# Performance work log

Measured on AMD Instinct MI355X. Metric: run time of the kernel, lower is better.

## Reference

```python
import jax, jax.numpy as jnp
import numpy as np

TOPK = 13
ALPHA = 1.0
BETA = 6.0
REG_MAX = 16
W_MATCH, W_IOU, W_DFL, W_CONTRAST = 1.0, 7.5, 1.5, 1.0
EPS = 1e-7


def bbox_iou(a, b):
    # a, b: [..., 4] xyxy, broadcastable
    x1 = jnp.maximum(a[..., 0], b[..., 0])
    y1 = jnp.maximum(a[..., 1], b[..., 1])
    x2 = jnp.minimum(a[..., 2], b[..., 2])
    y2 = jnp.minimum(a[..., 3], b[..., 3])
    inter = jnp.clip(x2 - x1, 0.0) * jnp.clip(y2 - y1, 0.0)
    area_a = (a[..., 2] - a[..., 0]) * (a[..., 3] - a[..., 1])
    area_b = (b[..., 2] - b[..., 0]) * (b[..., 3] - b[..., 1])
    return inter / (area_a + area_b - inter + EPS)


def bbox_ciou(a, b):
    iou = bbox_iou(a, b)
    cw = jnp.maximum(a[..., 2], b[..., 2]) - jnp.minimum(a[..., 0], b[..., 0])
    ch = jnp.maximum(a[..., 3], b[..., 3]) - jnp.minimum(a[..., 1], b[..., 1])
    c2 = cw * cw + ch * ch + EPS
    rho2 = ((b[..., 0] + b[..., 2] - a[..., 0] - a[..., 2]) ** 2
            + (b[..., 1] + b[..., 3] - a[..., 1] - a[..., 3]) ** 2) * 0.25
    w1, h1 = a[..., 2] - a[..., 0], a[..., 3] - a[..., 1] + EPS
    w2, h2 = b[..., 2] - b[..., 0], b[..., 3] - b[..., 1] + EPS
    v = (4.0 / (np.pi ** 2)) * (jnp.arctan(w2 / h2) - jnp.arctan(w1 / h1)) ** 2
    alpha = jax.lax.stop_gradient(v / (v - iou + (1.0 + EPS)))
    return iou - rho2 / c2 - v * alpha


def _per_image(scores, boxes, logits, prompt, gts, anchors, stride, img_size):
    # scores [N], boxes [N,4], logits [N,4*REG_MAX], prompt [D], gts [G,4]
    N = scores.shape[0]
    dt = scores.dtype
    inside = ((anchors[None, :, 0] >= gts[:, None, 0]) & (anchors[None, :, 0] <= gts[:, None, 2])
              & (anchors[None, :, 1] >= gts[:, None, 1]) & (anchors[None, :, 1] <= gts[:, None, 3]))  # [G,N]
    ious = bbox_iou(boxes[None, :, :], gts[:, None, :])  # [G,N]
    prob = jax.nn.sigmoid(scores)
    align = jnp.where(inside, jnp.power(prob[None, :], ALPHA) * jnp.power(ious, BETA), -1.0)  # [G,N]
    top_vals, top_idx = jax.lax.top_k(align, TOPK)  # [G,TOPK]
    metric = jax.vmap(lambda i, v: jnp.full((N,), -2.0, dt).at[i].set(v))(top_idx, top_vals)  # [G,N]
    best = metric.max(axis=0)
    matched = metric.argmax(axis=0)  # [N]
    fg = best >= 0.0  # valid candidates always have align >= 0
    fgf = fg.astype(dt)
    overlap = jnp.take_along_axis(ious, matched[None, :], axis=0)[0]  # [N]
    target_scores = jnp.where(fg, jnp.maximum(overlap, 0.1), 0.0)
    target_boxes = jnp.where(fg[:, None], gts[matched], 0.0)  # [N,4]
    n_pos = fgf.sum()
    denom = jnp.maximum(n_pos, 1.0)
    # ---- BCE-with-logits (mean over all anchors) ----
    bce = jnp.maximum(scores, 0.0) - scores * target_scores + jnp.log1p(jnp.exp(-jnp.abs(scores)))
    match_loss = bce.mean()
    # ---- CIoU loss (masked mean over positives) ----
    ciou = bbox_ciou(boxes, target_boxes)
    iou_loss = jnp.sum((1.0 - ciou) * fgf) / denom
    # ---- DFL ----
    dist = jnp.concatenate([anchors - target_boxes[:, :2], target_boxes[:, 2:] - anchors], axis=-1) / stride
    dist = jnp.clip(dist, 0.0, REG_MAX - 1 - 0.01)  # [N,4]
    logsm = jax.nn.log_softmax(logits.reshape(N, 4, REG_MAX), axis=-1)
    tl = dist.astype(jnp.int32)
    tr = jnp.minimum(tl + 1, REG_MAX - 1)
    wl = tr.astype(dt) - dist
    wr = 1.0 - wl
    ll = -jnp.take_along_axis(logsm, tl[..., None], axis=-1)[..., 0]
    lr = -jnp.take_along_axis(logsm, tr[..., None], axis=-1)[..., 0]
    dfl = ll * wl + lr * wr  # [N,4]
    dfl_loss = jnp.sum(dfl * fgf[:, None]) / (4.0 * denom)
    # ---- Contrastive prompt alignment ----
    center = (target_boxes[:, :2] + target_boxes[:, 2:]) * 0.5 / jnp.maximum(img_size, 1.0)
    cv = center / jnp.maximum(jnp.linalg.norm(center, axis=-1, keepdims=True), 1e-12)
    pv = prompt[:2]
    pv = pv / jnp.maximum(jnp.linalg.norm(pv), 1e-12)
    contrast_loss = jnp.sum((1.0 - jnp.sum(cv * pv[None, :], axis=-1)) * fgf) / denom
    # ---- stats ----
    pos_score_sum = jnp.sum(prob * fgf)
    neg_score_sum = jnp.sum(prob * (1.0 - fgf))
    matched_iou_sum = jnp.sum(overlap * fgf)
    return match_loss, iou_loss, dfl_loss, contrast_loss, n_pos, pos_score_sum, neg_score_sum, matched_iou_sum


def setup_inputs() -> dict:
    img = 1280
    pts, strs = [], []
    for s in (8, 16, 32):
        n = img // s
        xs = (np.arange(n, dtype=np.float32) + 0.5) * s
        gx, gy = np.meshgrid(xs, xs)
        pts.append(np.stack([gx.ravel(), gy.ravel()], -1))
        strs.append(np.full((n * n, 1), s, np.float32))
    anchor_points = jnp.asarray(np.concatenate(pts).astype(np.float32))  # [33600,2]
    stride_tensor = jnp.asarray(np.concatenate(strs))  # [33600,1]
    N = anchor_points.shape[0]
    B, G = 16, 20
    k = jax.random.split(jax.random.key(0), 6)
    pred_scores = jax.random.normal(k[0], (B, N), jnp.float32) - 2.0
    off = jax.random.uniform(k[1], (B, N, 4), jnp.float32, 4.0, 80.0)
    ap = anchor_points[None, :, :]
    pred_boxes = jnp.concatenate([ap - off[..., :2], ap + off[..., 2:]], -1)
    box_distribution = jax.random.normal(k[2], (B, N, 4 * REG_MAX), jnp.float32)
    prompt_embedding = jax.random.normal(k[3], (B, 256), jnp.float32)
    c = jax.random.uniform(k[4], (B, G, 2), jnp.float32, 100.0, 1180.0)
    wh = jax.random.uniform(k[5], (B, G, 2), jnp.float32, 30.0, 300.0)
    gt_boxes = jnp.concatenate([c - wh * 0.5, c + wh * 0.5], -1)
    return {"pred_boxes": pred_boxes, "pred_scores": pred_scores, "anchor_points": anchor_points,
            "stride_tensor": stride_tensor, "box_distribution": box_distribution,
            "prompt_embedding": prompt_embedding, "gt_boxes": gt_boxes, "image_size": img}


def reference(pred_boxes, pred_scores, anchor_points, stride_tensor, box_distribution, prompt_embedding, gt_boxes, image_size):
    B, N = pred_scores.shape
    res = jax.vmap(_per_image, in_axes=(0, 0, 0, 0, 0, None, None, None))(
        pred_scores, pred_boxes, box_distribution, prompt_embedding, gt_boxes,
        anchor_points, stride_tensor, float(image_size))
    match, iou, dfl, contrast, n_pos, pos_sum, neg_sum, miou = [r.sum() for r in res]
    total_pos = n_pos
    total_neg = float(B * N) - total_pos
    nb = float(B)
    loss = (W_MATCH * match + W_IOU * iou + W_DFL * dfl + W_CONTRAST * contrast) / nb
    pd = jnp.maximum(total_pos, 1.0)
    nd = jnp.maximum(total_neg, 1.0)
    return (loss, match / nb, iou / nb, dfl / nb, contrast / nb,
            total_pos, total_neg, pos_sum / pd, neg_sum / nd, miou / pd)
```

## Files before the change

kernel.cpp:

```cpp
#include <hip/hip_runtime.h>
#include <math.h>

#define TOPK 13
#define REG_MAX 16
#define EPSF 1e-7f
#define MAXM 512
#define NEG_SENT -1e30f
#define NBCE 256

__global__ __launch_bounds__(256) void k1_kernel(
    const float* __restrict__ boxes,
    const float* __restrict__ scores,
    const float* __restrict__ gts,
    const int*   __restrict__ img_sz,
    unsigned long long* __restrict__ pk_out,
    float* __restrict__ bcepart,
    int N, int G, int NBG, int total)
{
    const int tid  = threadIdx.x;
    const int lane = tid & 63;
    const int w    = tid >> 6;

    if ((int)blockIdx.x >= NBG) {
        const int blk = blockIdx.x - NBG;
        float bce0 = 0.f, prsum = 0.f;
        const int nvec = total >> 2;
        const float4* s4 = (const float4*)scores;
        for (int n = blk*256 + tid; n < nvec; n += NBCE*256) {
            float4 v = s4[n];
            float ss[4] = { v.x, v.y, v.z, v.w };
#pragma unroll
            for (int q = 0; q < 4; q++) {
                float s = ss[q];
                bce0  += fmaxf(s, 0.0f) + log1pf(expf(-fabsf(s)));
                prsum += 1.0f / (1.0f + expf(-s));
            }
        }
        if (blk == 0) {
            for (int n = (nvec << 2) + tid; n < total; n += 256) {
                float s = scores[n];
                bce0  += fmaxf(s, 0.0f) + log1pf(expf(-fabsf(s)));
                prsum += 1.0f / (1.0f + expf(-s));
            }
        }
        float v1 = bce0, v2 = prsum;
#pragma unroll
        for (int off = 32; off > 0; off >>= 1) {
            v1 += __shfl_xor(v1, off);
            v2 += __shfl_xor(v2, off);
        }
        __shared__ float r1[4], r2[4];
        if (lane == 0) { r1[w] = v1; r2[w] = v2; }
        __syncthreads();
        if (tid == 0) {
            bcepart[blk*2 + 0] = r1[0] + r1[1] + r1[2] + r1[3];
            bcepart[blk*2 + 1] = r2[0] + r2[1] + r2[2] + r2[3];
        }
        return;
    }

    const int bg  = blockIdx.x;
    const int b   = bg / G;
    const int g   = bg - b * G;
    const int img = img_sz[0];

    const float4 gt = ((const float4*)gts)[bg];
    const float area_b = (gt.z - gt.x) * (gt.w - gt.y);

    float lv[TOPK];
    int   li[TOPK];
#pragma unroll
    for (int i = 0; i < TOPK; i++) { lv[i] = NEG_SENT; li[i] = 0; }

    const float4* bx = (const float4*)(boxes + (size_t)b * N * 4);
    const float*  sc = scores + (size_t)b * N;

    int base = 0;
#pragma unroll
    for (int L = 0; L < 3; L++) {
        const int s = 8 << L;
        const int n = img / s;
        const float fs = (float)s;
        int i0 = max(0,     (int)ceilf (gt.x / fs - 0.5f) - 1);
        int i1 = min(n - 1, (int)floorf(gt.z / fs - 0.5f) + 1);
        int j0 = max(0,     (int)ceilf (gt.y / fs - 0.5f) - 1);
        int j1 = min(n - 1, (int)floorf(gt.w / fs - 0.5f) + 1);
        if (i1 >= i0 && j1 >= j0) {
            const int W = i1 - i0 + 1;
            const int cnt = W * (j1 - j0 + 1);
            for (int t = tid; t < cnt; t += 256) {
                const int i = i0 + t % W;
                const int j = j0 + t / W;
                const int idx = base + j * n + i;
                const float4 a    = bx[idx];
                const float  sraw = sc[idx];
                const float ax = ((float)i + 0.5f) * fs;
                const float ay = ((float)j + 0.5f) * fs;
                float x1 = fmaxf(a.x, gt.x), y1 = fmaxf(a.y, gt.y);
                float x2 = fminf(a.z, gt.z), y2 = fminf(a.w, gt.w);
                float inter  = fmaxf(x2 - x1, 0.0f) * fmaxf(y2 - y1, 0.0f);
                float area_a = (a.z - a.x) * (a.w - a.y);
                float iou  = inter / (area_a + area_b - inter + EPSF);
                float prob = 1.0f / (1.0f + expf(-sraw));
                float i2 = iou * iou;
                float align = prob * i2 * i2 * i2;
                bool inside = (ax >= gt.x) & (ax <= gt.z) & (ay >= gt.y) & (ay <= gt.w);
                align = inside ? align : NEG_SENT;
                if (align > lv[TOPK-1]) {
                    float cv = align; int ci = idx;
#pragma unroll
                    for (int q = 0; q < TOPK; q++) {
                        if (cv > lv[q]) {
                            float tv = lv[q]; int ti = li[q];
                            lv[q] = cv; li[q] = ci; cv = tv; ci = ti;
                        }
                    }
                }
            }
        }
        base += n * n;
    }

    __shared__ float sval[256 * TOPK];
    __shared__ int   sidx[256 * TOPK];
#pragma unroll
    for (int i = 0; i < TOPK; i++) { sval[tid*TOPK+i] = lv[i]; sidx[tid*TOPK+i] = li[i]; }
    __builtin_amdgcn_s_waitcnt(0);

    __shared__ float wtv[4][TOPK];
    __shared__ int   wti[4][TOPK];
    int h = 0;
    for (int k = 0; k < TOPK; k++) {
        float v = (h < TOPK) ? sval[tid*TOPK + h] : NEG_SENT;
        float bv = v; int bs = lane;
#pragma unroll
        for (int off = 32; off > 0; off >>= 1) {
            float ov = __shfl_xor(bv, off);
            int   os = __shfl_xor(bs, off);
            if (ov > bv || (ov == bv && os < bs)) { bv = ov; bs = os; }
        }
        if (lane == bs) {
            wtv[w][k] = v;
            wti[w][k] = sidx[tid*TOPK + h];
            h++;
        }
    }
    __syncthreads();

    if (w == 0) {
        int hh = 0;
        for (int k = 0; k < TOPK; k++) {
            float v = (lane < 4) ? wtv[lane & 3][hh] : NEG_SENT;
            float bv = v; int bs = lane;
#pragma unroll
            for (int off = 32; off > 0; off >>= 1) {
                float ov = __shfl_xor(bv, off);
                int   os = __shfl_xor(bs, off);
                if (ov > bv || (ov == bv && os < bs)) { bv = ov; bs = os; }
            }
            if (lane == bs) {
                unsigned long long p = 0ull;
                if (v >= 0.0f) {
                    p = (1ull << 62)
                      | ((unsigned long long)(unsigned int)wti[lane & 3][hh] << 37)
                      | ((unsigned long long)__float_as_uint(v) << 5)
                      | (unsigned long long)(31 - g);
                }
                pk_out[bg*TOPK + k] = p;
                hh++;
            }
        }
    }
}

__global__ __launch_bounds__(64) void fg_kernel(
    const float* __restrict__ boxes, const float* __restrict__ scores,
    const float* __restrict__ logits, const float* __restrict__ prompt,
    const float* __restrict__ gts, const int* __restrict__ img_sz,
    const unsigned long long* __restrict__ pk_in,
    float* __restrict__ part, int N, int G, int PD)
{
    const int bg   = blockIdx.x;
    const int b    = bg / G;
    const int g    = bg - b * G;
    const int lane = threadIdx.x;
    const int M    = G * TOPK;

    __shared__ unsigned long long pk[MAXM];
    for (int e = lane; e < M; e += 64) pk[e] = pk_in[b*M + e];
    __builtin_amdgcn_s_waitcnt(0);

    const int ent = lane >> 2;
    const int q   = lane & 3;
    unsigned long long mine = 0ull;
    if (ent < TOPK) mine = pk[g*TOPK + ent];

    int lose = 0;
    if (mine != 0ull) {
        for (int e2 = q; e2 < M; e2 += 4) {
            unsigned long long p2 = pk[e2];
            lose |= (int)((((p2 ^ mine) >> 37) == 0ull) & (p2 > mine));
        }
    }
    lose |= __shfl_xor(lose, 1);
    lose |= __shfl_xor(lose, 2);
    const bool winner = (mine != 0ull) && (lose == 0);

    const float4 tb = ((const float4*)gts)[b*G + g];
    const int img = img_sz[0];

    float side = 0.f;
    float npos = 0.f, iouv = 0.f, conv = 0.f, probv = 0.f, corrv = 0.f, miouv = 0.f;

    if (winner) {
        const int idx = (int)((mine >> 37) & 0x1FFFFFFull);
        const int n0 = img >> 3, n1 = img >> 4, n2 = img >> 5;
        int r = idx; float fs; int n;
        if (r < n0*n0)                 { fs = 8.0f;  n = n0; }
        else if (r < n0*n0 + n1*n1)    { r -= n0*n0;         fs = 16.0f; n = n1; }
        else                           { r -= n0*n0 + n1*n1; fs = 32.0f; n = n2; }
        (void)n2;
        const int jj = r / n, ii = r - jj * n;
        const float ax = ((float)ii + 0.5f) * fs;
        const float ay = ((float)jj + 0.5f) * fs;

        float dq = (q == 0) ? (ax - tb.x) : (q == 1) ? (ay - tb.y)
                 : (q == 2) ? (tb.z - ax) : (tb.w - ay);
        dq /= fs;
        const float4* lg4 = (const float4*)(logits + ((size_t)b*N + idx) * (4*REG_MAX)) + q*4;
        float4 q0 = lg4[0], q1 = lg4[1], q2 = lg4[2], q3 = lg4[3];
        float row[REG_MAX] = { q0.x,q0.y,q0.z,q0.w, q1.x,q1.y,q1.z,q1.w,
                               q2.x,q2.y,q2.z,q2.w, q3.x,q3.y,q3.z,q3.w };
        float d = fminf(fmaxf(dq, 0.0f), (float)(REG_MAX-1) - 0.01f);
        int tl = (int)d;
        int tr = min(tl + 1, REG_MAX - 1);
        float wl = (float)tr - d;
        float wr = 1.0f - wl;
        float m = row[0];
#pragma unroll
        for (int jx = 1; jx < REG_MAX; jx++) m = fmaxf(m, row[jx]);
        float se = 0.f, rtl = row[0], rtr = row[0];
#pragma unroll
        for (int jx = 0; jx < REG_MAX; jx++) {
            se += expf(row[jx] - m);
            rtl = (jx == tl) ? row[jx] : rtl;
            rtr = (jx == tr) ? row[jx] : rtr;
        }
        float lse = m + logf(se);
        side = (lse - rtl) * wl + (lse - rtr) * wr;
    }
    float dfl4 = side;
    dfl4 += __shfl_xor(dfl4, 1);
    dfl4 += __shfl_xor(dfl4, 2);

    float dflv = 0.f;
    if (winner && q == 0) {
        const int idx = (int)((mine >> 37) & 0x1FFFFFFull);
        const float4 a = ((const float4*)(boxes + (size_t)b*N*4))[idx];
        float s    = scores[(size_t)b*N + idx];
        float prob = 1.0f / (1.0f + expf(-s));

        float x1 = fmaxf(a.x, tb.x), y1 = fmaxf(a.y, tb.y);
        float x2 = fminf(a.z, tb.z), y2 = fminf(a.w, tb.w);
        float inter  = fmaxf(x2 - x1, 0.f) * fmaxf(y2 - y1, 0.f);
        float area_a = (a.z - a.x) * (a.w - a.y);
        float area_b = (tb.z - tb.x) * (tb.w - tb.y);
        float iou = inter / (area_a + area_b - inter + EPSF);
        float tsc = fmaxf(iou, 0.1f);

        float cw = fmaxf(a.z, tb.z) - fminf(a.x, tb.x);
        float ch = fmaxf(a.w, tb.w) - fminf(a.y, tb.y);
        float c2 = cw*cw + ch*ch + EPSF;
        float dxc = tb.x + tb.z - a.x - a.z;
        float dyc = tb.y + tb.w - a.y - a.w;
        float rho2 = (dxc*dxc + dyc*dyc) * 0.25f;
        float w1 = a.z - a.x, h1 = a.w - a.y + EPSF;
        float w2 = tb.z - tb.x, h2 = tb.w - tb.y + EPSF;
        float dat = atanf(w2/h2) - atanf(w1/h1);
        float v   = 0.4052847345693511f * dat * dat;
        float alpha = v / (v - iou + (1.0f + EPSF));
        float ciou  = iou - rho2/c2 - v*alpha;
        iouv = 1.0f - ciou;
        dflv = dfl4;

        float imgf = fmaxf((float)img, 1.0f);
        float p0 = prompt[(size_t)b*PD + 0], p1 = prompt[(size_t)b*PD + 1];
        float pn = fmaxf(sqrtf(p0*p0 + p1*p1), 1e-12f);
        float cx = (tb.x + tb.z) * 0.5f / imgf;
        float cy = (tb.y + tb.w) * 0.5f / imgf;
        float cn = fmaxf(sqrtf(cx*cx + cy*cy), 1e-12f);
        conv = 1.0f - (cx*(p0/pn) + cy*(p1/pn)) / cn;

        npos  = 1.0f;
        probv = prob;
        corrv = -s * tsc;
        miouv = iou;
    }

    float vals[7] = { npos, iouv, dflv, conv, probv, corrv, miouv };
#pragma unroll
    for (int k = 0; k < 7; k++) {
        float v = vals[k];
#pragma unroll
        for (int off = 32; off > 0; off >>= 1) v += __shfl_xor(v, off);
        vals[k] = v;
    }
    if (lane == 0) {
        float* p = part + (size_t)bg * 7;
#pragma unroll
        for (int k = 0; k < 7; k++) p[k] = vals[k];
    }
}

__global__ __launch_bounds__(64) void finalize_kernel(
    const float* __restrict__ part, const float* __restrict__ bcepart,
    float* __restrict__ out, int N, int B, int G)
{
    const int lane = threadIdx.x;
    float np = 0.f, iouS = 0.f, dflS = 0.f, conS = 0.f;
    float probS = 0.f, corrS = 0.f, miouS = 0.f;
    if (lane < B) {
        float a0=0,a1=0,a2=0,a3=0,a4=0,a5=0,a6=0;
        const float* p = part + (size_t)lane * G * 7;
        for (int g = 0; g < G; g++) {
            a0 += p[g*7+0]; a1 += p[g*7+1]; a2 += p[g*7+2]; a3 += p[g*7+3];
            a4 += p[g*7+4]; a5 += p[g*7+5]; a6 += p[g*7+6];
        }
        float denom = fmaxf(a0, 1.0f);
        np    = a0;
        iouS  = a1 / denom;
        dflS  = a2 / (4.0f * denom);
        conS  = a3 / denom;
        probS = a4;
        corrS = a5;
        miouS = a6;
    }
    float b0 = 0.f, b1 = 0.f;
    for (int qb = lane; qb < NBCE; qb += 64) {
        b0 += bcepart[2*qb + 0];
        b1 += bcepart[2*qb + 1];
    }
    float vals[9] = { np, iouS, dflS, conS, probS, corrS, miouS, b0, b1 };
#pragma unroll
    for (int k = 0; k < 9; k++) {
        float v = vals[k];
#pragma unroll
        for (int off = 32; off > 0; off >>= 1) v += __shfl_xor(v, off);
        vals[k] = v;
    }
    if (lane == 0) {
        float bce0 = vals[7], prall = vals[8];
        float match = (bce0 + vals[5]) / (float)N;
        float iou = vals[1], dfl = vals[2], con = vals[3];
        float tp  = vals[0];
        float tn  = (float)B * (float)N - tp;
        float nb  = (float)B;
        float loss = (1.0f*match + 7.5f*iou + 1.5f*dfl + 1.0f*con) / nb;
        float pd = fmaxf(tp, 1.0f), nd = fmaxf(tn, 1.0f);
        out[0] = loss;
        out[1] = match / nb;
        out[2] = iou / nb;
        out[3] = dfl / nb;
        out[4] = con / nb;
        out[5] = tp;
        out[6] = tn;
        out[7] = vals[4] / pd;
        out[8] = (prall - vals[4]) / nd;
        out[9] = vals[6] / pd;
    }
}

extern "C" void kernel_launch(void* const* d_in, const int* in_sizes, int n_in,
                              void* d_out, int out_size, void* d_ws, size_t ws_size,
                              hipStream_t stream)
{
    const float* boxes   = (const float*)d_in[0];
    const float* scores  = (const float*)d_in[1];
    const float* logits  = (const float*)d_in[4];
    const float* prompt  = (const float*)d_in[5];
    const float* gts     = (const float*)d_in[6];
    const int*   img     = (const int*)d_in[7];

    const int N  = in_sizes[2] / 2;
    const int B  = in_sizes[1] / N;
    const int G  = in_sizes[6] / (B * 4);
    const int PD = in_sizes[5] / B;
    const int NBG = B * G;

    float* out = (float*)d_out;
    char*  ws  = (char*)d_ws;

    unsigned long long* pk = (unsigned long long*)ws;
    size_t off = (size_t)NBG * TOPK * sizeof(unsigned long long);
    off = (off + 63) & ~(size_t)63;
    float* part = (float*)(ws + off);
    off += (size_t)NBG * 7 * sizeof(float);
    off = (off + 63) & ~(size_t)63;
    float* bcep = (float*)(ws + off);

    k1_kernel<<<NBG + NBCE, 256, 0, stream>>>(boxes, scores, gts, img,
                                              pk, bcep, N, G, NBG, B*N);
    fg_kernel<<<NBG, 64, 0, stream>>>(boxes, scores, logits, prompt,
                                      gts, img, pk, part, N, G, PD);
    finalize_kernel<<<1, 64, 0, stream>>>(part, bcep, out, N, B, G);
}
```

Before: 227.7 us.

## Fuse TAL top-k and foreground loss into one per-image kernel

Replaces the per-(image,GT) top-k kernel and the separate foreground-loss kernel with a single kernel that runs one block per image. Each wavefront handles a subset of GTs and keeps its candidates in shared memory, then the block resolves conflicts and computes the CIoU, DFL and contrast terms for all winners in place. This removes a kernel launch and the global round trip of the packed candidates. In exchange, parallelism drops from B*G blocks to B blocks, each wave walks its GTs serially, and the conflict check becomes an O(M^2) loop per thread. G is assumed to be at most 32.

```diff
diff --git a/kernel.cpp b/kernel.cpp
--- a/kernel.cpp
+++ b/kernel.cpp
@@ -4,25 +4,32 @@
 #define TOPK 13
 #define REG_MAX 16
 #define EPSF 1e-7f
-#define MAXM 512
 #define NEG_SENT -1e30f
 #define NBCE 256
-
-__global__ __launch_bounds__(256) void k1_kernel(
+#define MAXG 32
+
+__global__ __launch_bounds__(256) void mega_kernel(
     const float* __restrict__ boxes,
     const float* __restrict__ scores,
+    const float* __restrict__ logits,
+    const float* __restrict__ prompt,
     const float* __restrict__ gts,
     const int*   __restrict__ img_sz,
-    unsigned long long* __restrict__ pk_out,
-    float* __restrict__ bcepart,
-    int N, int G, int NBG, int total)
+    float* __restrict__ ws_img,
+    float* __restrict__ ws_bce,
+    int N, int B, int G, int PD, int total)
 {
     const int tid  = threadIdx.x;
     const int lane = tid & 63;
     const int w    = tid >> 6;
 
-    if ((int)blockIdx.x >= NBG) {
-        const int blk = blockIdx.x - NBG;
+    __shared__ float sval[256 * TOPK];
+    __shared__ int   sidx[256 * TOPK];
+    __shared__ unsigned long long pk[MAXG * TOPK];
+    __shared__ float wred[4][7];
+
+    if ((int)blockIdx.x >= B) {
+        const int blk = blockIdx.x - B;
         float bce0 = 0.f, prsum = 0.f;
         const int nvec = total >> 2;
         const float4* s4 = (const float4*)scores;
@@ -49,108 +56,88 @@
             v1 += __shfl_xor(v1, off);
             v2 += __shfl_xor(v2, off);
         }
-        __shared__ float r1[4], r2[4];
-        if (lane == 0) { r1[w] = v1; r2[w] = v2; }
+        if (lane == 0) { wred[w][0] = v1; wred[w][1] = v2; }
         __syncthreads();
         if (tid == 0) {
-            bcepart[blk*2 + 0] = r1[0] + r1[1] + r1[2] + r1[3];
-            bcepart[blk*2 + 1] = r2[0] + r2[1] + r2[2] + r2[3];
+            ws_bce[blk*2 + 0] = wred[0][0] + wred[1][0] + wred[2][0] + wred[3][0];
+            ws_bce[blk*2 + 1] = wred[0][1] + wred[1][1] + wred[2][1] + wred[3][1];
         }
         return;
     }
 
-    const int bg  = blockIdx.x;
-    const int b   = bg / G;
-    const int g   = bg - b * G;
+    const int b   = blockIdx.x;
     const int img = img_sz[0];
-
-    const float4 gt = ((const float4*)gts)[bg];
-    const float area_b = (gt.z - gt.x) * (gt.w - gt.y);
-
-    float lv[TOPK];
-    int   li[TOPK];
-#pragma unroll
-    for (int i = 0; i < TOPK; i++) { lv[i] = NEG_SENT; li[i] = 0; }
+    const int M   = G * TOPK;
 
     const float4* bx = (const float4*)(boxes + (size_t)b * N * 4);
     const float*  sc = scores + (size_t)b * N;
 
-    int base = 0;
-#pragma unroll
-    for (int L = 0; L < 3; L++) {
-        const int s = 8 << L;
-        const int n = img / s;
-        const float fs = (float)s;
-        int i0 = max(0,     (int)ceilf (gt.x / fs - 0.5f) - 1);
-        int i1 = min(n - 1, (int)floorf(gt.z / fs - 0.5f) + 1);
-        int j0 = max(0,     (int)ceilf (gt.y / fs - 0.5f) - 1);
-        int j1 = min(n - 1, (int)floorf(gt.w / fs - 0.5f) + 1);
-        if (i1 >= i0 && j1 >= j0) {
-            const int W = i1 - i0 + 1;
-            const int cnt = W * (j1 - j0 + 1);
-            for (int t = tid; t < cnt; t += 256) {
-                const int i = i0 + t % W;
-                const int j = j0 + t / W;
-                const int idx = base + j * n + i;
-                const float4 a    = bx[idx];
-                const float  sraw = sc[idx];
-                const float ax = ((float)i + 0.5f) * fs;
-                const float ay = ((float)j + 0.5f) * fs;
-                float x1 = fmaxf(a.x, gt.x), y1 = fmaxf(a.y, gt.y);
-                float x2 = fminf(a.z, gt.z), y2 = fminf(a.w, gt.w);
-                float inter  = fmaxf(x2 - x1, 0.0f) * fmaxf(y2 - y1, 0.0f);
-                float area_a = (a.z - a.x) * (a.w - a.y);
-                float iou  = inter / (area_a + area_b - inter + EPSF);
-                float prob = 1.0f / (1.0f + expf(-sraw));
-                float i2 = iou * iou;
-                float align = prob * i2 * i2 * i2;
-                bool inside = (ax >= gt.x) & (ax <= gt.z) & (ay >= gt.y) & (ay <= gt.w);
-                align = inside ? align : NEG_SENT;
-                if (align > lv[TOPK-1]) {
-                    float cv = align; int ci = idx;
-#pragma unroll
-                    for (int q = 0; q < TOPK; q++) {
-                        if (cv > lv[q]) {
-                            float tv = lv[q]; int ti = li[q];
-                            lv[q] = cv; li[q] = ci; cv = tv; ci = ti;
+    for (int g = w; g < G; g += 4) {
+        const float4 gt = ((const float4*)gts)[b*G + g];
+        const float area_b = (gt.z - gt.x) * (gt.w - gt.y);
+
+        float lv[TOPK];
+        int   li[TOPK];
+#pragma unroll
+        for (int i = 0; i < TOPK; i++) { lv[i] = NEG_SENT; li[i] = 0; }
+
+        int base = 0;
+#pragma unroll
+        for (int L = 0; L < 3; L++) {
+            const int s = 8 << L;
+            const int n = img / s;
+            const float fs = (float)s;
+            int i0 = max(0,     (int)ceilf (gt.x / fs - 0.5f) - 1);
+            int i1 = min(n - 1, (int)floorf(gt.z / fs - 0.5f) + 1);
+            int j0 = max(0,     (int)ceilf (gt.y / fs - 0.5f) - 1);
+            int j1 = min(n - 1, (int)floorf(gt.w / fs - 0.5f) + 1);
+            if (i1 >= i0 && j1 >= j0) {
+                const int W = i1 - i0 + 1;
+                const int cnt = W * (j1 - j0 + 1);
+                const int q64 = 64 / W, r64 = 64 - q64 * W;
+                int ii = lane % W, jj = lane / W;
+                for (int t = lane; t < cnt; t += 64) {
+                    const int i = i0 + ii;
+                    const int j = j0 + jj;
+                    const int idx = base + j * n + i;
+                    const float4 a    = bx[idx];
+                    const float  sraw = sc[idx];
+                    const float ax = ((float)i + 0.5f) * fs;
+                    const float ay = ((float)j + 0.5f) * fs;
+                    float x1 = fmaxf(a.x, gt.x), y1 = fmaxf(a.y, gt.y);
+                    float x2 = fminf(a.z, gt.z), y2 = fminf(a.w, gt.w);
+                    float inter  = fmaxf(x2 - x1, 0.0f) * fmaxf(y2 - y1, 0.0f);
+                    float area_a = (a.z - a.x) * (a.w - a.y);
+                    float iou  = inter / (area_a + area_b - inter + EPSF);
+                    float prob = 1.0f / (1.0f + expf(-sraw));
+                    float i2v = iou * iou;
+                    float align = prob * i2v * i2v * i2v;
+                    bool inside = (ax >= gt.x) & (ax <= gt.z) & (ay >= gt.y) & (ay <= gt.w);
+                    align = inside ? align : NEG_SENT;
+                    if (align > lv[TOPK-1]) {
+                        float cv = align; int ci = idx;
+#pragma unroll
+                        for (int q = 0; q < TOPK; q++) {
+                            if (cv > lv[q]) {
+                                float tv = lv[q]; int ti = li[q];
+                                lv[q] = cv; li[q] = ci; cv = tv; ci = ti;
+                            }
                         }
                     }
+                    ii += r64; jj += q64;
+                    if (ii >= W) { ii -= W; jj++; }
                 }
             }
-        }
-        base += n * n;
-    }
-
-    __shared__ float sval[256 * TOPK];
-    __shared__ int   sidx[256 * TOPK];
-#pragma unroll
-    for (int i = 0; i < TOPK; i++) { sval[tid*TOPK+i] = lv[i]; sidx[tid*TOPK+i] = li[i]; }
-    __builtin_amdgcn_s_waitcnt(0);
-
-    __shared__ float wtv[4][TOPK];
-    __shared__ int   wti[4][TOPK];
-    int h = 0;
-    for (int k = 0; k < TOPK; k++) {
-        float v = (h < TOPK) ? sval[tid*TOPK + h] : NEG_SENT;
-        float bv = v; int bs = lane;
-#pragma unroll
-        for (int off = 32; off > 0; off >>= 1) {
-            float ov = __shfl_xor(bv, off);
-            int   os = __shfl_xor(bs, off);
-            if (ov > bv || (ov == bv && os < bs)) { bv = ov; bs = os; }
-        }
-        if (lane == bs) {
-            wtv[w][k] = v;
-            wti[w][k] = sidx[tid*TOPK + h];
-            h++;
-        }
-    }
-    __syncthreads();
-
-    if (w == 0) {
-        int hh = 0;
+            base += n * n;
+        }
+
+#pragma unroll
+        for (int i = 0; i < TOPK; i++) { sval[tid*TOPK+i] = lv[i]; sidx[tid*TOPK+i] = li[i]; }
+        __builtin_amdgcn_s_waitcnt(0);
+
+        int h = 0;
         for (int k = 0; k < TOPK; k++) {
-            float v = (lane < 4) ? wtv[lane & 3][hh] : NEG_SENT;
+            float v = (h < TOPK) ? sval[tid*TOPK + h] : NEG_SENT;
             float bv = v; int bs = lane;
 #pragma unroll
             for (int off = 32; off > 0; off >>= 1) {
@@ -162,102 +149,50 @@
                 unsigned long long p = 0ull;
                 if (v >= 0.0f) {
                     p = (1ull << 62)
-                      | ((unsigned long long)(unsigned int)wti[lane & 3][hh] << 37)
+                      | ((unsigned long long)(unsigned int)sidx[tid*TOPK + h] << 37)
                       | ((unsigned long long)__float_as_uint(v) << 5)
                       | (unsigned long long)(31 - g);
                 }
-                pk_out[bg*TOPK + k] = p;
-                hh++;
-            }
-        }
-    }
-}
-
-__global__ __launch_bounds__(64) void fg_kernel(
-    const float* __restrict__ boxes, const float* __restrict__ scores,
-    const float* __restrict__ logits, const float* __restrict__ prompt,
-    const float* __restrict__ gts, const int* __restrict__ img_sz,
-    const unsigned long long* __restrict__ pk_in,
-    float* __restrict__ part, int N, int G, int PD)
-{
-    const int bg   = blockIdx.x;
-    const int b    = bg / G;
-    const int g    = bg - b * G;
-    const int lane = threadIdx.x;
-    const int M    = G * TOPK;
-
-    __shared__ unsigned long long pk[MAXM];
-    for (int e = lane; e < M; e += 64) pk[e] = pk_in[b*M + e];
-    __builtin_amdgcn_s_waitcnt(0);
-
-    const int ent = lane >> 2;
-    const int q   = lane & 3;
-    unsigned long long mine = 0ull;
-    if (ent < TOPK) mine = pk[g*TOPK + ent];
-
-    int lose = 0;
-    if (mine != 0ull) {
-        for (int e2 = q; e2 < M; e2 += 4) {
+                pk[g*TOPK + k] = p;
+                h++;
+            }
+        }
+    }
+    __syncthreads();
+
+    float npos = 0.f, iouS = 0.f, dflS = 0.f, conS = 0.f;
+    float probS = 0.f, corrS = 0.f, miouS = 0.f;
+
+    const float imgf = fmaxf((float)img, 1.0f);
+    float p0 = prompt[(size_t)b*PD + 0], p1 = prompt[(size_t)b*PD + 1];
+    float pn = fmaxf(sqrtf(p0*p0 + p1*p1), 1e-12f);
+    p0 /= pn; p1 /= pn;
+
+    for (int e = tid; e < M; e += 256) {
+        const unsigned long long mine = pk[e];
+        if (mine == 0ull) continue;
+        bool lose = false;
+        for (int e2 = 0; e2 < M; e2++) {
             unsigned long long p2 = pk[e2];
-            lose |= (int)((((p2 ^ mine) >> 37) == 0ull) & (p2 > mine));
-        }
-    }
-    lose |= __shfl_xor(lose, 1);
-    lose |= __shfl_xor(lose, 2);
-    const bool winner = (mine != 0ull) && (lose == 0);
-
-    const float4 tb = ((const float4*)gts)[b*G + g];
-    const int img = img_sz[0];
-
-    float side = 0.f;
-    float npos = 0.f, iouv = 0.f, conv = 0.f, probv = 0.f, corrv = 0.f, miouv = 0.f;
-
-    if (winner) {
+            lose |= (((p2 ^ mine) >> 37) == 0ull) & (p2 > mine);
+        }
+        if (lose) continue;
+
+        const int g   = e / TOPK;
         const int idx = (int)((mine >> 37) & 0x1FFFFFFull);
-        const int n0 = img >> 3, n1 = img >> 4, n2 = img >> 5;
+        const float4 tb = ((const float4*)gts)[b*G + g];
+
+        const int n0 = img >> 3, n1 = img >> 4;
         int r = idx; float fs; int n;
-        if (r < n0*n0)                 { fs = 8.0f;  n = n0; }
-        else if (r < n0*n0 + n1*n1)    { r -= n0*n0;         fs = 16.0f; n = n1; }
-        else                           { r -= n0*n0 + n1*n1; fs = 32.0f; n = n2; }
-        (void)n2;
+        if (r < n0*n0)              { fs = 8.0f;  n = n0; }
+        else if (r < n0*n0 + n1*n1) { r -= n0*n0;         fs = 16.0f; n = n1; }
+        else                        { r -= n0*n0 + n1*n1; fs = 32.0f; n = img >> 5; }
         const int jj = r / n, ii = r - jj * n;
         const float ax = ((float)ii + 0.5f) * fs;
         const float ay = ((float)jj + 0.5f) * fs;
 
-        float dq = (q == 0) ? (ax - tb.x) : (q == 1) ? (ay - tb.y)
-                 : (q == 2) ? (tb.z - ax) : (tb.w - ay);
-        dq /= fs;
-        const float4* lg4 = (const float4*)(logits + ((size_t)b*N + idx) * (4*REG_MAX)) + q*4;
-        float4 q0 = lg4[0], q1 = lg4[1], q2 = lg4[2], q3 = lg4[3];
-        float row[REG_MAX] = { q0.x,q0.y,q0.z,q0.w, q1.x,q1.y,q1.z,q1.w,
-                               q2.x,q2.y,q2.z,q2.w, q3.x,q3.y,q3.z,q3.w };
-        float d = fminf(fmaxf(dq, 0.0f), (float)(REG_MAX-1) - 0.01f);
-        int tl = (int)d;
-        int tr = min(tl + 1, REG_MAX - 1);
-        float wl = (float)tr - d;
-        float wr = 1.0f - wl;
-        float m = row[0];
-#pragma unroll
-        for (int jx = 1; jx < REG_MAX; jx++) m = fmaxf(m, row[jx]);
-        float se = 0.f, rtl = row[0], rtr = row[0];
-#pragma unroll
-        for (int jx = 0; jx < REG_MAX; jx++) {
-            se += expf(row[jx] - m);
-            rtl = (jx == tl) ? row[jx] : rtl;
-            rtr = (jx == tr) ? row[jx] : rtr;
-        }
-        float lse = m + logf(se);
-        side = (lse - rtl) * wl + (lse - rtr) * wr;
-    }
-    float dfl4 = side;
-    dfl4 += __shfl_xor(dfl4, 1);
-    dfl4 += __shfl_xor(dfl4, 2);
-
-    float dflv = 0.f;
-    if (winner && q == 0) {
-        const int idx = (int)((mine >> 37) & 0x1FFFFFFull);
-        const float4 a = ((const float4*)(boxes + (size_t)b*N*4))[idx];
-        float s    = scores[(size_t)b*N + idx];
+        const float4 a = bx[idx];
+        float s    = sc[idx];
         float prob = 1.0f / (1.0f + expf(-s));
 
         float x1 = fmaxf(a.x, tb.x), y1 = fmaxf(a.y, tb.y);
@@ -280,24 +215,49 @@
         float v   = 0.4052847345693511f * dat * dat;
         float alpha = v / (v - iou + (1.0f + EPSF));
         float ciou  = iou - rho2/c2 - v*alpha;
-        iouv = 1.0f - ciou;
-        dflv = dfl4;
-
-        float imgf = fmaxf((float)img, 1.0f);
-        float p0 = prompt[(size_t)b*PD + 0], p1 = prompt[(size_t)b*PD + 1];
-        float pn = fmaxf(sqrtf(p0*p0 + p1*p1), 1e-12f);
+        iouS += 1.0f - ciou;
+
+        float d4[4] = { (ax - tb.x)/fs, (ay - tb.y)/fs,
+                        (tb.z - ax)/fs, (tb.w - ay)/fs };
+        const float4* lg4 = (const float4*)(logits + ((size_t)b*N + idx) * (4*REG_MAX));
+        float dfl_n = 0.f;
+#pragma unroll
+        for (int sd = 0; sd < 4; sd++) {
+            float4 q0 = lg4[sd*4+0], q1 = lg4[sd*4+1], q2 = lg4[sd*4+2], q3 = lg4[sd*4+3];
+            float row[REG_MAX] = { q0.x,q0.y,q0.z,q0.w, q1.x,q1.y,q1.z,q1.w,
+                                   q2.x,q2.y,q2.z,q2.w, q3.x,q3.y,q3.z,q3.w };
+            float d = fminf(fmaxf(d4[sd], 0.0f), (float)(REG_MAX-1) - 0.01f);
+            int tl = (int)d;
+            int tr = min(tl + 1, REG_MAX - 1);
+            float wl = (float)tr - d;
+            float wr = 1.0f - wl;
+            float m = row[0];
+#pragma unroll
+            for (int jx = 1; jx < REG_MAX; jx++) m = fmaxf(m, row[jx]);
+            float se = 0.f, rtl = row[0], rtr = row[0];
+#pragma unroll
+            for (int jx = 0; jx < REG_MAX; jx++) {
+                se += expf(row[jx] - m);
+                rtl = (jx == tl) ? row[jx] : rtl;
+                rtr = (jx == tr) ? row[jx] : rtr;
+            }
+            float lse = m + logf(se);
+            dfl_n += (lse - rtl) * wl + (lse - rtr) * wr;
+        }
+        dflS += dfl_n;
+
         float cx = (tb.x + tb.z) * 0.5f / imgf;
         float cy = (tb.y + tb.w) * 0.5f / imgf;
         float cn = fmaxf(sqrtf(cx*cx + cy*cy), 1e-12f);
-        conv = 1.0f - (cx*(p0/pn) + cy*(p1/pn)) / cn;
-
-        npos  = 1.0f;
-        probv = prob;
-        corrv = -s * tsc;
-        miouv = iou;
-    }
-
-    float vals[7] = { npos, iouv, dflv, conv, probv, corrv, miouv };
+        conS += 1.0f - (cx*p0 + cy*p1) / cn;
+
+        npos  += 1.0f;
+        probS += prob;
+        corrS += -s * tsc;
+        miouS += iou;
+    }
+
+    float vals[7] = { npos, iouS, dflS, conS, probS, corrS, miouS };
 #pragma unroll
     for (int k = 0; k < 7; k++) {
         float v = vals[k];
@@ -306,41 +266,43 @@
         vals[k] = v;
     }
     if (lane == 0) {
-        float* p = part + (size_t)bg * 7;
-#pragma unroll
-        for (int k = 0; k < 7; k++) p[k] = vals[k];
+#pragma unroll
+        for (int k = 0; k < 7; k++) wred[w][k] = vals[k];
+    }
+    __syncthreads();
+    if (tid == 0) {
+        float fin[7];
+#pragma unroll
+        for (int k = 0; k < 7; k++)
+            fin[k] = wred[0][k] + wred[1][k] + wred[2][k] + wred[3][k];
+        float np    = fin[0];
+        float denom = fmaxf(np, 1.0f);
+        float* p = ws_img + (size_t)b * 8;
+        p[0] = np;
+        p[1] = fin[1] / denom;
+        p[2] = fin[2] / (4.0f * denom);
+        p[3] = fin[3] / denom;
+        p[4] = fin[4];
+        p[5] = fin[5];
+        p[6] = fin[6];
     }
 }
 
 __global__ __launch_bounds__(64) void finalize_kernel(
-    const float* __restrict__ part, const float* __restrict__ bcepart,
-    float* __restrict__ out, int N, int B, int G)
+    const float* __restrict__ ws_img, const float* __restrict__ ws_bce,
+    float* __restrict__ out, int N, int B)
 {
     const int lane = threadIdx.x;
-    float np = 0.f, iouS = 0.f, dflS = 0.f, conS = 0.f;
-    float probS = 0.f, corrS = 0.f, miouS = 0.f;
+    float vals[9] = {0,0,0,0,0,0,0,0,0};
     if (lane < B) {
-        float a0=0,a1=0,a2=0,a3=0,a4=0,a5=0,a6=0;
-        const float* p = part + (size_t)lane * G * 7;
-        for (int g = 0; g < G; g++) {
-            a0 += p[g*7+0]; a1 += p[g*7+1]; a2 += p[g*7+2]; a3 += p[g*7+3];
-            a4 += p[g*7+4]; a5 += p[g*7+5]; a6 += p[g*7+6];
-        }
-        float denom = fmaxf(a0, 1.0f);
-        np    = a0;
-        iouS  = a1 / denom;
-        dflS  = a2 / (4.0f * denom);
-        conS  = a3 / denom;
-        probS = a4;
-        corrS = a5;
-        miouS = a6;
-    }
-    float b0 = 0.f, b1 = 0.f;
+        const float* p = ws_img + (size_t)lane * 8;
+#pragma unroll
+        for (int k = 0; k < 7; k++) vals[k] = p[k];
+    }
     for (int qb = lane; qb < NBCE; qb += 64) {
-        b0 += bcepart[2*qb + 0];
-        b1 += bcepart[2*qb + 1];
-    }
-    float vals[9] = { np, iouS, dflS, conS, probS, corrS, miouS, b0, b1 };
+        vals[7] += ws_bce[2*qb + 0];
+        vals[8] += ws_bce[2*qb + 1];
+    }
 #pragma unroll
     for (int k = 0; k < 9; k++) {
         float v = vals[k];
@@ -385,22 +347,16 @@
     const int B  = in_sizes[1] / N;
     const int G  = in_sizes[6] / (B * 4);
     const int PD = in_sizes[5] / B;
-    const int NBG = B * G;
 
     float* out = (float*)d_out;
     char*  ws  = (char*)d_ws;
 
-    unsigned long long* pk = (unsigned long long*)ws;
-    size_t off = (size_t)NBG * TOPK * sizeof(unsigned long long);
-    off = (off + 63) & ~(size_t)63;
-    float* part = (float*)(ws + off);
-    off += (size_t)NBG * 7 * sizeof(float);
-    off = (off + 63) & ~(size_t)63;
-    float* bcep = (float*)(ws + off);
-
-    k1_kernel<<<NBG + NBCE, 256, 0, stream>>>(boxes, scores, gts, img,
-                                              pk, bcep, N, G, NBG, B*N);
-    fg_kernel<<<NBG, 64, 0, stream>>>(boxes, scores, logits, prompt,
-                                      gts, img, pk, part, N, G, PD);
-    finalize_kernel<<<1, 64, 0, stream>>>(part, bcep, out, N, B, G);
+    float* ws_img = (float*)ws;
+    size_t off = ((size_t)B * 8 * sizeof(float) + 63) & ~(size_t)63;
+    float* ws_bce = (float*)(ws + off);
+
+    mega_kernel<<<B + NBCE, 256, 0, stream>>>(boxes, scores, logits, prompt,
+                                              gts, img, ws_img, ws_bce,
+                                              N, B, G, PD, B*N);
+    finalize_kernel<<<1, 64, 0, stream>>>(ws_img, ws_bce, out, N, B);
 }
```

Measured after the change: 375.9 us. +65.1%, slower.
